# Optimization experiments

Measured on AMD Instinct MI355X. Metric: run time of the kernel, lower is better.

The kernel has to match this reference:

```python
import jax, jax.numpy as jnp
import numpy as np

D_MODEL = 1024
N_HEADS = 16
D_HEAD = D_MODEL // N_HEADS
D_FF = 4096
BATCH = 2
SEQ = 2048
EPS = 1e-5


def setup_inputs() -> dict:
    key = jax.random.key(0)
    ks = jax.random.split(key, 8)
    s = 0.02
    x = jax.random.normal(ks[0], (BATCH, SEQ, D_MODEL), dtype=jnp.float32)
    # Per-head projection weights, stacked: [H, d_head, d_model] (torch Linear stores (out,in))
    wq = jax.random.normal(ks[1], (N_HEADS, D_HEAD, D_MODEL), dtype=jnp.float32) * s
    wk = jax.random.normal(ks[2], (N_HEADS, D_HEAD, D_MODEL), dtype=jnp.float32) * s
    wv = jax.random.normal(ks[3], (N_HEADS, D_HEAD, D_MODEL), dtype=jnp.float32) * s
    wo = jax.random.normal(ks[4], (D_MODEL, D_MODEL), dtype=jnp.float32) * s
    w1 = jax.random.normal(ks[5], (D_FF, D_MODEL), dtype=jnp.float32) * s
    w2 = jax.random.normal(ks[6], (D_MODEL, D_FF), dtype=jnp.float32) * s
    ln1_g = jnp.ones((D_MODEL,), jnp.float32)
    ln1_b = jnp.zeros((D_MODEL,), jnp.float32)
    ln2_g = jnp.ones((D_MODEL,), jnp.float32)
    ln2_b = jnp.zeros((D_MODEL,), jnp.float32)
    return {"x": x, "wq": wq, "wk": wk, "wv": wv, "wo": wo,
            "w1": w1, "w2": w2, "ln1_g": ln1_g, "ln1_b": ln1_b,
            "ln2_g": ln2_g, "ln2_b": ln2_b}


def _layer_norm(x, g, b):
    mu = jnp.mean(x, axis=-1, keepdims=True)
    var = jnp.mean(jnp.square(x - mu), axis=-1, keepdims=True)
    return (x - mu) * jax.lax.rsqrt(var + EPS) * g + b


def _mha(h, wq, wk, wv, wo):
    # h: [b,s,d]; wq/wk/wv: [H,dh,d] -> q/k/v: [b,H,s,dh]
    q = jnp.einsum('bsd,hed->bhse', h, wq)
    k = jnp.einsum('bsd,hed->bhse', h, wk)
    v = jnp.einsum('bsd,hed->bhse', h, wv)
    scores = jnp.einsum('bhqe,bhke->bhqk', q, k) / jnp.sqrt(jnp.float32(D_HEAD))
    weights = jax.nn.softmax(scores, axis=-1)
    ctx = jnp.einsum('bhqk,bhke->bhqe', weights, v)  # [b,H,s,dh]
    # concat heads in order (head 0 first) -> [b,s,H*dh]
    concat = jnp.transpose(ctx, (0, 2, 1, 3)).reshape(h.shape[0], h.shape[1], D_MODEL)
    return concat @ wo.T


def reference(x, wq, wk, wv, wo, w1, w2, ln1_g, ln1_b, ln2_g, ln2_b):
    h = _layer_norm(x, ln1_g, ln1_b)
    attn_out = _mha(h, wq, wk, wv, wo)
    h2 = _layer_norm(x + attn_out, ln2_g, ln2_b)
    ff = jax.nn.gelu(h2 @ w1.T, approximate=False) @ w2.T
    return x + ff
```

## Files before the change

kernel.cpp:

```cpp
#include <hip/hip_runtime.h>
#include <hip/hip_bf16.h>
#include <math.h>

typedef __bf16 bf16_t;
typedef __bf16 bf16x8 __attribute__((ext_vector_type(8)));
typedef __bf16 bf16x4 __attribute__((ext_vector_type(4)));
typedef float f32x4 __attribute__((ext_vector_type(4)));
typedef unsigned int u32;
typedef u32 u32x2 __attribute__((ext_vector_type(2)));

#define DM 1024
#define SEQL 2048
#define NTOK 4096
#define QKVN 3072

__device__ __forceinline__ void gload_lds16(const bf16_t* g, bf16_t* l){
  __builtin_amdgcn_global_load_lds((const __attribute__((address_space(1))) void*)g,
                                   (__attribute__((address_space(3))) void*)l, 16, 0, 0);
}
__device__ __forceinline__ u32 ldsoff(const void* p){
  return (u32)(size_t)(__attribute__((address_space(3))) const void*)p;
}
__device__ __forceinline__ u32x2 tr64(u32 byte_off){
  u32x2 d;
  asm volatile("ds_read_b64_tr_b16 %0, %1" : "=v"(d) : "v"(byte_off));
  return d;
}
__device__ __forceinline__ u32 pack2(float a, float b){
  union{ __bf16 h[2]; u32 w; } z;
  z.h[0]=(__bf16)a; z.h[1]=(__bf16)b; return z.w;
}

__global__ __launch_bounds__(256) void prep_kernel(
    const float* __restrict__ wq, const float* __restrict__ wk,
    const float* __restrict__ wv, const float* __restrict__ wo,
    const float* __restrict__ w1, const float* __restrict__ w2,
    const float* __restrict__ x,  const float* __restrict__ g1,
    const float* __restrict__ b1,
    bf16_t* __restrict__ wqkv_b, bf16_t* __restrict__ wo_b,
    bf16_t* __restrict__ w1_b,   bf16_t* __restrict__ w2_b,
    bf16_t* __restrict__ h1)
{
  __shared__ float red[8];
  const int bid = blockIdx.x;
  const int t = threadIdx.x;
  if (bid < 12288){
    const int flat = (bid*256 + t)*4;
    const int seg = flat >> 20;
    const int off1m = flat & 1048575;
    const float* src; bf16_t* dst;
    if (seg < 3){
      src = (seg==0 ? wq : (seg==1 ? wk : wv)) + off1m;
      dst = wqkv_b + flat;
    } else if (seg == 3){
      src = wo + off1m;  dst = wo_b + off1m;
    } else if (seg < 8){
      src = w1 + (flat - 4*1048576);  dst = w1_b + (flat - 4*1048576);
    } else {
      src = w2 + (flat - 8*1048576);  dst = w2_b + (flat - 8*1048576);
    }
    const float4 v = *(const float4*)src;
    bf16x4 o; o[0]=(__bf16)v.x; o[1]=(__bf16)v.y; o[2]=(__bf16)v.z; o[3]=(__bf16)v.w;
    *(bf16x4*)dst = o;
  } else {
    const int row = bid - 12288;
    const float4 v = *(const float4*)(x + (size_t)row*DM + t*4);
    float s  = v.x+v.y+v.z+v.w;
    float sq = v.x*v.x+v.y*v.y+v.z*v.z+v.w*v.w;
    #pragma unroll
    for (int m=1;m<64;m<<=1){ s += __shfl_xor(s,m); sq += __shfl_xor(sq,m); }
    const int w = t>>6;
    if ((t&63)==0){ red[w]=s; red[4+w]=sq; }
    __syncthreads();
    s  = red[0]+red[1]+red[2]+red[3];
    sq = red[4]+red[5]+red[6]+red[7];
    const float mean = s*(1.f/DM);
    const float var  = sq*(1.f/DM) - mean*mean;
    const float rstd = rsqrtf(var + 1e-5f);
    const float4 gg = *(const float4*)(g1 + t*4);
    const float4 bb = *(const float4*)(b1 + t*4);
    bf16x4 o;
    o[0]=(__bf16)((v.x-mean)*rstd*gg.x+bb.x);
    o[1]=(__bf16)((v.y-mean)*rstd*gg.y+bb.y);
    o[2]=(__bf16)((v.z-mean)*rstd*gg.z+bb.z);
    o[3]=(__bf16)((v.w-mean)*rstd*gg.w+bb.w);
    *(bf16x4*)(h1 + (size_t)row*DM + t*4) = o;
  }
}

__global__ __launch_bounds__(256) void ln_kernel(const float* __restrict__ in,
    const float* __restrict__ g, const float* __restrict__ bta,
    bf16_t* __restrict__ outp)
{
  const int row = blockIdx.x;
  const int t = threadIdx.x;
  const float4 v = *(const float4*)(in + (size_t)row*DM + t*4);
  float s  = v.x+v.y+v.z+v.w;
  float sq = v.x*v.x+v.y*v.y+v.z*v.z+v.w*v.w;
  #pragma unroll
  for (int m=1;m<64;m<<=1){ s += __shfl_xor(s,m); sq += __shfl_xor(sq,m); }
  __shared__ float red[8];
  const int w = t>>6;
  if ((t&63)==0){ red[w]=s; red[4+w]=sq; }
  __syncthreads();
  s  = red[0]+red[1]+red[2]+red[3];
  sq = red[4]+red[5]+red[6]+red[7];
  const float mean = s*(1.f/DM);
  const float var  = sq*(1.f/DM) - mean*mean;
  const float rstd = rsqrtf(var + 1e-5f);
  const float4 gg = *(const float4*)(g + t*4);
  const float4 bb = *(const float4*)(bta + t*4);
  bf16x4 o;
  o[0]=(__bf16)((v.x-mean)*rstd*gg.x+bb.x);
  o[1]=(__bf16)((v.y-mean)*rstd*gg.y+bb.y);
  o[2]=(__bf16)((v.z-mean)*rstd*gg.z+bb.z);
  o[3]=(__bf16)((v.w-mean)*rstd*gg.w+bb.w);
  *(bf16x4*)(outp + (size_t)row*DM + t*4) = o;
}

template<int EPI>
__global__ __launch_bounds__(512, 2) void gemm8ph(
    const bf16_t* __restrict__ A, const bf16_t* __restrict__ Bw,
    void* __restrict__ Cout, int N, int K)
{
  __shared__ __align__(16) char ldsb[131072];
  const int tid = threadIdx.x, lane = tid&63, wid = tid>>6;
  const int q16 = lane&15, g = lane>>4;
  const int wm = wid>>2, wn = wid&3;

  const int flat = blockIdx.y*gridDim.x + blockIdx.x;
  const int xcd = flat&7, jj = flat>>3;
  const int NY = gridDim.y;
  const int jdiv = jj/NY, jmod = jj - jdiv*NY;
  const int bm = (xcd*2 + jdiv)*256, bn = jmod*256;

  int mloc, kloc;
  {
    const u32 L = tid*16;
    const u32 logical = L ^ (((L>>9)&1)<<5);
    mloc = (int)(logical>>6);
    kloc = (int)((logical&63)>>1);
  }
  const bf16_t* asrc = A  + (size_t)(bm + mloc)*K + kloc;
  const bf16_t* bsrc = Bw + (size_t)(bn + mloc)*K + kloc;
  const u32 laneOff = ((u32)(q16*64 + g*16)) ^ ((u32)(q16&8)<<2);

  f32x4 acc[8][4] = {};
  bf16x8 bv[4];

  auto stage = [&](int buf, int kh, int isB, int s){
    const bf16_t* src = isB ? bsrc : asrc;
    #pragma unroll
    for (int h2=0; h2<2; h2++)
      gload_lds16(src + (size_t)(h2*128)*K + s*64 + kh*32,
                  (bf16_t*)(ldsb + buf*65536 + isB*32768 + kh*16384 + h2*8192 + tid*16));
  };

  stage(0,0,0,0); stage(0,0,1,0); stage(0,1,0,0); stage(0,1,1,0);
  stage(1,0,0,1); stage(1,0,1,1);
  asm volatile("s_waitcnt vmcnt(4)" ::: "memory");
  __builtin_amdgcn_s_barrier();

  const int NSTEP = K>>6;
  const int NIT = NSTEP>>1;

#define PHASE(BUF,KH,MH,DOST,SBUF,SKH,SISB,SSTEP,CK) { \
    bf16x8 av[4]; \
    const char* Ab_ = ldsb + (BUF)*65536 + (KH)*16384 + wm*8192; \
    _Pragma("unroll") for (int jx=0;jx<4;jx++) \
      av[jx] = *(const bf16x8*)(Ab_ + (((MH)*4+jx)<<10) + laneOff); \
    if ((MH)==0){ \
      const char* Bb_ = ldsb + (BUF)*65536 + 32768 + (KH)*16384 + (wn>>1)*8192; \
      _Pragma("unroll") for (int jx=0;jx<4;jx++) \
        bv[jx] = *(const bf16x8*)(Bb_ + ((((wn&1)*4)+jx)<<10) + laneOff); \
    } \
    if (DOST) stage(SBUF,SKH,SISB,SSTEP); \
    asm volatile("s_barrier" ::: "memory"); \
    asm volatile("s_waitcnt lgkmcnt(0)" ::: "memory"); \
    __builtin_amdgcn_s_setprio(1); \
    _Pragma("unroll") for (int jx=0;jx<4;jx++) \
      _Pragma("unroll") for (int j2=0;j2<4;j2++) \
        acc[(MH)*4+jx][j2] = __builtin_amdgcn_mfma_f32_16x16x32_bf16(av[jx], bv[j2], acc[(MH)*4+jx][j2],0,0,0); \
    __builtin_amdgcn_s_setprio(0); \
    if (CK){ if (nl) { asm volatile("s_waitcnt vmcnt(4)" ::: "memory"); } \
             else    { asm volatile("s_waitcnt vmcnt(0)" ::: "memory"); } } \
    asm volatile("s_barrier" ::: "memory"); }

  for (int it=0; it<NIT; it++){
    const int s0 = 2*it, s1 = s0+1;
    const bool nl = (it+1 < NIT);
    PHASE(0,0,0, 1,  1,1,0, s1,   0)
    PHASE(0,0,1, 1,  1,1,1, s1,   0)
    PHASE(0,1,0, nl, 0,0,0, s0+2, 0)
    PHASE(0,1,1, nl, 0,0,1, s0+2, 1)
    PHASE(1,0,0, nl, 0,1,0, s0+2, 0)
    PHASE(1,0,1, nl, 0,1,1, s0+2, 0)
    PHASE(1,1,0, nl, 1,0,0, s1+2, 0)
    PHASE(1,1,1, nl, 1,0,1, s1+2, 1)
  }
#undef PHASE

  #pragma unroll
  for (int fm=0; fm<8; fm++)
    #pragma unroll
    for (int fn=0; fn<4; fn++)
      #pragma unroll
      for (int i=0; i<4; i++){
        const int r = bm + wm*128 + fm*16 + g*4 + i;
        const int c = bn + wn*64 + fn*16 + q16;
        const size_t idx = (size_t)r*N + c;
        const float vv = acc[fm][fn][i];
        if constexpr (EPI==0){
          ((bf16_t*)Cout)[idx] = (__bf16)vv;
        } else {
          const float ge = 0.5f*vv*(1.0f + erff(vv*0.70710678118654752f));
          ((bf16_t*)Cout)[idx] = (__bf16)ge;
        }
      }
}

__global__ __launch_bounds__(512, 2) void gemm128(
    const bf16_t* __restrict__ A, const bf16_t* __restrict__ Bw,
    float* __restrict__ Cout, const float* __restrict__ X,
    int N, int K)
{
  constexpr int BK = 32;
  __shared__ __align__(16) char ldsb[3*16384];
  const int tid = threadIdx.x, lane = tid&63, wid = tid>>6;
  const int q16 = lane&15, g = lane>>4;
  const int wm = wid>>2, wn = wid&3;

  const int flat = blockIdx.y*gridDim.x + blockIdx.x;
  const int xcd = flat&7, j = flat>>3;
  const int bm = ((xcd<<2) + (j>>3))*128, bn = (j&7)*128;

  int mloc, kloc;
  {
    const u32 L = tid*16;
    const u32 logical = L ^ (((L>>9)&1)<<5);
    mloc = (int)(logical>>6);
    kloc = (int)((logical&63)>>1);
  }
  const bf16_t* asrc = A  + (size_t)(bm + mloc)*K + kloc;
  const bf16_t* bsrc = Bw + (size_t)(bn + mloc)*K + kloc;
  const u32 laneOff = ((u32)(q16*64 + g*16)) ^ ((u32)(q16&8)<<2);

  f32x4 acc[4][2] = {};

  auto stageA = [&](int buf, int k0){
    gload_lds16(asrc + k0, (bf16_t*)(ldsb + buf*16384 + tid*16));
  };
  auto stageB = [&](int buf, int k0){
    gload_lds16(bsrc + k0, (bf16_t*)(ldsb + buf*16384 + 8192 + tid*16));
  };

  stageA(0,0); stageB(0,0);
  stageA(1,BK); stageB(1,BK);
  asm volatile("s_waitcnt vmcnt(2)" ::: "memory");
  __builtin_amdgcn_s_barrier();

  const int NT = K/BK;
  int bcur = 0;
  for (int kt=0; kt<NT; kt++){
    const int bstg = (bcur >= 1) ? bcur-1 : bcur+2;
    const char* Ab = ldsb + bcur*16384 + wm*4096;
    const char* Bb = ldsb + bcur*16384 + 8192 + wn*2048;
    const bool sOK = (kt+2 < NT);
    const int k0s = (kt+2)*BK;
    bf16x8 bv[2];
    #pragma unroll
    for (int p=0; p<2; p++){
      bf16x8 av[2];
      #pragma unroll
      for (int jx=0;jx<2;jx++)
        av[jx] = *(const bf16x8*)(Ab + ((p*2+jx)<<10) + laneOff);
      if (p==0){
        #pragma unroll
        for (int jx=0;jx<2;jx++)
          bv[jx] = *(const bf16x8*)(Bb + (jx<<10) + laneOff);
      }
      if (sOK){
        if (p==0) stageA(bstg,k0s);
        else      stageB(bstg,k0s);
      }
      asm volatile("s_barrier" ::: "memory");
      __builtin_amdgcn_s_setprio(1);
      #pragma unroll
      for (int jx=0;jx<2;jx++)
        #pragma unroll
        for (int j2=0;j2<2;j2++)
          acc[p*2+jx][j2] = __builtin_amdgcn_mfma_f32_16x16x32_bf16(av[jx], bv[j2], acc[p*2+jx][j2], 0,0,0);
      __builtin_amdgcn_s_setprio(0);
      if (p==1){
        if (sOK) asm volatile("s_waitcnt vmcnt(2)" ::: "memory");
        else     asm volatile("s_waitcnt vmcnt(0)" ::: "memory");
      }
      asm volatile("s_barrier" ::: "memory");
    }
    bcur = (bcur==2)?0:bcur+1;
  }

  #pragma unroll
  for (int fm=0; fm<4; fm++)
    #pragma unroll
    for (int fn=0; fn<2; fn++)
      #pragma unroll
      for (int i=0; i<4; i++){
        const int r = bm + wm*64 + fm*16 + g*4 + i;
        const int c = bn + wn*32 + fn*16 + q16;
        const size_t idx = (size_t)r*N + c;
        Cout[idx] = X[idx] + acc[fm][fn][i];
      }
}

__global__ __launch_bounds__(512, 4) void attn_kernel(
    const bf16_t* __restrict__ QKV, bf16_t* __restrict__ Ctx)
{
  __shared__ __align__(16) bf16_t Ks[2][64*64];
  __shared__ __align__(16) bf16_t Vs[2][16*4*72];
  const int tid = threadIdx.x, lane = tid&63, w = tid>>6;
  const int g = lane>>4, q16 = lane&15;
  const int bh = blockIdx.y, b = bh>>4, h = bh&15;
  const int qr0 = blockIdx.x*128 + w*16;
  const size_t tok0 = (size_t)b*SEQL;
  const int ch0 = h*64;

  bf16x8 aq[2];
  #pragma unroll
  for (int ks=0; ks<2; ks++){
    bf16x8 t = *(const bf16x8*)(QKV + (tok0+qr0+q16)*QKVN + ch0 + ks*32 + g*8);
    #pragma unroll
    for (int jx=0;jx<8;jx++) t[jx] = (__bf16)((float)t[jx]*0.125f);
    aq[ks] = t;
  }

  const int srow = tid>>3, sc8 = (tid&7)*8;
  const bf16_t* kptr = QKV + (tok0+srow)*QKVN + 1024 + ch0 + sc8;
  const bf16_t* vptr = kptr + 1024;
  const int kwoff = srow*64 + (sc8 ^ ((srow&7)<<3));
  const int vwoff = ((srow>>2)*4 + (sc8>>4))*72 + (srow&3)*16 + (sc8&15);

  float mrun = -1e30f, lrun = 0.f;
  f32x4 o[4] = {};

  bf16x8 kreg = *(const bf16x8*)kptr;
  bf16x8 vreg = *(const bf16x8*)vptr;
  *(bf16x8*)&Ks[0][kwoff] = kreg;
  *(bf16x8*)&Vs[0][vwoff] = vreg;
  kreg = *(const bf16x8*)(kptr + (size_t)64*QKVN);
  vreg = *(const bf16x8*)(vptr + (size_t)64*QKVN);

  const int NT = SEQL/64;
  for (int t=0; t<NT; t++){
    __syncthreads();
    if (t+1 < NT){
      *(bf16x8*)&Ks[(t+1)&1][kwoff] = kreg;
      *(bf16x8*)&Vs[(t+1)&1][vwoff] = vreg;
      if (t+2 < NT){
        kreg = *(const bf16x8*)(kptr + (size_t)(t+2)*64*QKVN);
        vreg = *(const bf16x8*)(vptr + (size_t)(t+2)*64*QKVN);
      }
    }
    const bf16_t* ksb = Ks[t&1];
    const u32 vs0 = ldsoff(&Vs[t&1][0]);

    f32x4 s[4] = {};
    #pragma unroll
    for (int ks=0; ks<2; ks++){
      #pragma unroll
      for (int fn=0; fn<4; fn++){
        const int r = fn*16 + q16;
        const int ce = ks*32 + g*8;
        bf16x8 bk = *(const bf16x8*)&ksb[r*64 + (ce ^ ((r&7)<<3))];
        s[fn] = __builtin_amdgcn_mfma_f32_16x16x32_bf16(bk, aq[ks], s[fn], 0, 0, 0);
      }
    }

    float m0 = fmaxf(fmaxf(s[0][0],s[0][1]), fmaxf(s[0][2],s[0][3]));
    float m1 = fmaxf(fmaxf(s[1][0],s[1][1]), fmaxf(s[1][2],s[1][3]));
    float m2 = fmaxf(fmaxf(s[2][0],s[2][1]), fmaxf(s[2][2],s[2][3]));
    float m3 = fmaxf(fmaxf(s[3][0],s[3][1]), fmaxf(s[3][2],s[3][3]));
    float mx = fmaxf(fmaxf(m0,m1), fmaxf(m2,m3));
    mx = fmaxf(mx, __shfl_xor(mx,16));
    mx = fmaxf(mx, __shfl_xor(mx,32));

    if (!__all(mx <= mrun + 8.0f)){
      const float mnew = fmaxf(mrun, mx);
      const float alpha = __expf(mrun - mnew);
      #pragma unroll
      for (int i=0;i<4;i++){
        const float ai = __shfl(alpha, g*4+i);
        o[0][i]*=ai; o[1][i]*=ai; o[2][i]*=ai; o[3][i]*=ai;
      }
      lrun *= alpha;
      mrun = mnew;
    }

    float rs = 0.f;
    u32 u[4][2];
    #pragma unroll
    for (int fn=0; fn<4; fn++){
      const float e0=__expf(s[fn][0]-mrun), e1=__expf(s[fn][1]-mrun);
      const float e2=__expf(s[fn][2]-mrun), e3=__expf(s[fn][3]-mrun);
      rs += (e0+e1)+(e2+e3);
      u[fn][0] = pack2(e0,e1);
      u[fn][1] = pack2(e2,e3);
    }
    rs += __shfl_xor(rs,16);
    rs += __shfl_xor(rs,32);
    lrun += rs;

    #pragma unroll
    for (int ks=0; ks<2; ks++){
      u32x2 vlo[4], vhi[4];
      #pragma unroll
      for (int ne=0; ne<4; ne++){
        const u32 vb = vs0 + (u32)((((ks*8 + 2*g)*4 + ne)*72 + q16)*2);
        vlo[ne] = tr64(vb);
        vhi[ne] = tr64(vb + 576);
      }
      union { u32 wd[4]; bf16x8 v; } pa;
      #pragma unroll
      for (int jj=0; jj<4; jj++){
        const int src = q16 + ((((g&1)<<1) + (jj>>1))<<4);
        const u32 a0 = (u32)__shfl((int)u[2*ks  ][jj&1], src);
        const u32 a1 = (u32)__shfl((int)u[2*ks+1][jj&1], src);
        pa.wd[jj] = (g&2) ? a1 : a0;
      }
      asm volatile("s_waitcnt lgkmcnt(0)" ::: "memory");
      __builtin_amdgcn_sched_barrier(0);
      union { u32x2 u2[2]; bf16x8 v; } cc;
      #pragma unroll
      for (int ne=0; ne<4; ne++){
        cc.u2[0]=vlo[ne]; cc.u2[1]=vhi[ne];
        o[ne] = __builtin_amdgcn_mfma_f32_16x16x32_bf16(pa.v, cc.v, o[ne], 0, 0, 0);
      }
    }
  }

  const float rl = 1.0f/lrun;
  #pragma unroll
  for (int i=0; i<4; i++){
    const float ri = __shfl(rl, g*4+i);
    #pragma unroll
    for (int ne=0; ne<4; ne++){
      const int r = qr0 + g*4 + i;
      Ctx[(tok0+r)*DM + ch0 + ne*16 + q16] = (__bf16)(o[ne][i]*ri);
    }
  }
}

extern "C" void kernel_launch(void* const* d_in, const int* in_sizes, int n_in,
                              void* d_out, int out_size, void* d_ws, size_t ws_size,
                              hipStream_t stream)
{
  (void)in_sizes; (void)n_in; (void)out_size; (void)ws_size;
  const float* x  = (const float*)d_in[0];
  const float* wq = (const float*)d_in[1];
  const float* wk = (const float*)d_in[2];
  const float* wv = (const float*)d_in[3];
  const float* wo = (const float*)d_in[4];
  const float* w1 = (const float*)d_in[5];
  const float* w2 = (const float*)d_in[6];
  const float* g1 = (const float*)d_in[7];
  const float* b1 = (const float*)d_in[8];
  const float* g2 = (const float*)d_in[9];
  const float* b2 = (const float*)d_in[10];
  float* out = (float*)d_out;
  char* ws = (char*)d_ws;
  const size_t MB = 1024ull*1024ull;

  bf16_t* wqkv_b = (bf16_t*)(ws);
  bf16_t* wo_b   = (bf16_t*)(ws + 6*MB);
  bf16_t* w1_b   = (bf16_t*)(ws + 8*MB);
  bf16_t* w2_b   = (bf16_t*)(ws + 16*MB);
  bf16_t* h1     = (bf16_t*)(ws + 24*MB);
  bf16_t* qkv    = (bf16_t*)(ws + 32*MB);
  bf16_t* ctx    = (bf16_t*)(ws + 56*MB);
  float*  res2   = (float*)(ws + 64*MB);
  bf16_t* h2     = h1;
  bf16_t* ffm    = (bf16_t*)(ws + 32*MB);

  prep_kernel<<<16384, 256, 0, stream>>>(wq, wk, wv, wo, w1, w2, x, g1, b1,
                                         wqkv_b, wo_b, w1_b, w2_b, h1);
  gemm8ph<0><<<dim3(16, 12), 512, 0, stream>>>(h1, wqkv_b, (void*)qkv, QKVN, 1024);
  attn_kernel<<<dim3(16, 32), 512, 0, stream>>>(qkv, ctx);
  gemm128<<<dim3(32, 8), 512, 0, stream>>>(ctx, wo_b, res2, x, 1024, 1024);
  ln_kernel<<<NTOK, 256, 0, stream>>>(res2, g2, b2, h2);
  gemm8ph<2><<<dim3(16, 16), 512, 0, stream>>>(h2, w1_b, (void*)ffm, 4096, 1024);
  gemm128<<<dim3(32, 8), 512, 0, stream>>>(ffm, w2_b, out, x, 1024, 4096);
}
```

Before: 247.2 us.

## Store residual in bf16, load K tiles via direct LDS DMA, use exp2 softmax

The out-projection GEMM now writes the residual sum x+attn as bf16, and the second layernorm reads bf16, which halves that intermediate's memory traffic. The attention kernel moves K tiles with global_load_lds straight into pre-swizzled LDS instead of staging them in registers. It also folds log2(e) into the Q scale so the softmax can use exp2f, with the rescale threshold adjusted to match. The cost is bf16 rounding of the residual before LN2, which slightly lowers accuracy.

```diff
diff --git a/kernel.cpp b/kernel.cpp
--- a/kernel.cpp
+++ b/kernel.cpp
@@ -88,13 +88,15 @@
   }
 }
 
-__global__ __launch_bounds__(256) void ln_kernel(const float* __restrict__ in,
+__global__ __launch_bounds__(256) void lnb_kernel(const bf16_t* __restrict__ in,
     const float* __restrict__ g, const float* __restrict__ bta,
     bf16_t* __restrict__ outp)
 {
   const int row = blockIdx.x;
   const int t = threadIdx.x;
-  const float4 v = *(const float4*)(in + (size_t)row*DM + t*4);
+  const bf16x4 raw = *(const bf16x4*)(in + (size_t)row*DM + t*4);
+  float4 v;
+  v.x=(float)raw[0]; v.y=(float)raw[1]; v.z=(float)raw[2]; v.w=(float)raw[3];
   float s  = v.x+v.y+v.z+v.w;
   float sq = v.x*v.x+v.y*v.y+v.z*v.z+v.w*v.w;
   #pragma unroll
@@ -219,9 +221,10 @@
       }
 }
 
+template<int EPI>
 __global__ __launch_bounds__(512, 2) void gemm128(
     const bf16_t* __restrict__ A, const bf16_t* __restrict__ Bw,
-    float* __restrict__ Cout, const float* __restrict__ X,
+    void* __restrict__ Cout, const float* __restrict__ X,
     int N, int K)
 {
   constexpr int BK = 32;
@@ -309,7 +312,9 @@
         const int r = bm + wm*64 + fm*16 + g*4 + i;
         const int c = bn + wn*32 + fn*16 + q16;
         const size_t idx = (size_t)r*N + c;
-        Cout[idx] = X[idx] + acc[fm][fn][i];
+        const float vv = X[idx] + acc[fm][fn][i];
+        if constexpr (EPI==0) ((bf16_t*)Cout)[idx] = (__bf16)vv;
+        else                  ((float*)Cout)[idx] = vv;
       }
 }
 
@@ -330,36 +335,31 @@
   for (int ks=0; ks<2; ks++){
     bf16x8 t = *(const bf16x8*)(QKV + (tok0+qr0+q16)*QKVN + ch0 + ks*32 + g*8);
     #pragma unroll
-    for (int jx=0;jx<8;jx++) t[jx] = (__bf16)((float)t[jx]*0.125f);
+    for (int jx=0;jx<8;jx++) t[jx] = (__bf16)((float)t[jx]*0.18033688f);
     aq[ks] = t;
   }
 
   const int srow = tid>>3, sc8 = (tid&7)*8;
-  const bf16_t* kptr = QKV + (tok0+srow)*QKVN + 1024 + ch0 + sc8;
-  const bf16_t* vptr = kptr + 1024;
-  const int kwoff = srow*64 + (sc8 ^ ((srow&7)<<3));
+  const bf16_t* kptr_swz = QKV + (tok0+srow)*QKVN + 1024 + ch0 + (sc8 ^ ((srow&7)<<3));
+  const bf16_t* vptr = QKV + (tok0+srow)*QKVN + 2048 + ch0 + sc8;
   const int vwoff = ((srow>>2)*4 + (sc8>>4))*72 + (srow&3)*16 + (sc8&15);
 
   float mrun = -1e30f, lrun = 0.f;
   f32x4 o[4] = {};
 
-  bf16x8 kreg = *(const bf16x8*)kptr;
+  gload_lds16(kptr_swz, &Ks[0][tid*8]);
   bf16x8 vreg = *(const bf16x8*)vptr;
-  *(bf16x8*)&Ks[0][kwoff] = kreg;
   *(bf16x8*)&Vs[0][vwoff] = vreg;
-  kreg = *(const bf16x8*)(kptr + (size_t)64*QKVN);
   vreg = *(const bf16x8*)(vptr + (size_t)64*QKVN);
 
   const int NT = SEQL/64;
   for (int t=0; t<NT; t++){
     __syncthreads();
     if (t+1 < NT){
-      *(bf16x8*)&Ks[(t+1)&1][kwoff] = kreg;
+      gload_lds16(kptr_swz + (size_t)(t+1)*64*QKVN, &Ks[(t+1)&1][tid*8]);
       *(bf16x8*)&Vs[(t+1)&1][vwoff] = vreg;
-      if (t+2 < NT){
-        kreg = *(const bf16x8*)(kptr + (size_t)(t+2)*64*QKVN);
+      if (t+2 < NT)
         vreg = *(const bf16x8*)(vptr + (size_t)(t+2)*64*QKVN);
-      }
     }
     const bf16_t* ksb = Ks[t&1];
     const u32 vs0 = ldsoff(&Vs[t&1][0]);
@@ -384,9 +384,9 @@
     mx = fmaxf(mx, __shfl_xor(mx,16));
     mx = fmaxf(mx, __shfl_xor(mx,32));
 
-    if (!__all(mx <= mrun + 8.0f)){
+    if (!__all(mx <= mrun + 11.54f)){
       const float mnew = fmaxf(mrun, mx);
-      const float alpha = __expf(mrun - mnew);
+      const float alpha = exp2f(mrun - mnew);
       #pragma unroll
       for (int i=0;i<4;i++){
         const float ai = __shfl(alpha, g*4+i);
@@ -400,8 +400,8 @@
     u32 u[4][2];
     #pragma unroll
     for (int fn=0; fn<4; fn++){
-      const float e0=__expf(s[fn][0]-mrun), e1=__expf(s[fn][1]-mrun);
-      const float e2=__expf(s[fn][2]-mrun), e3=__expf(s[fn][3]-mrun);
+      const float e0=exp2f(s[fn][0]-mrun), e1=exp2f(s[fn][1]-mrun);
+      const float e2=exp2f(s[fn][2]-mrun), e3=exp2f(s[fn][3]-mrun);
       rs += (e0+e1)+(e2+e3);
       u[fn][0] = pack2(e0,e1);
       u[fn][1] = pack2(e2,e3);
@@ -477,7 +477,7 @@
   bf16_t* h1     = (bf16_t*)(ws + 24*MB);
   bf16_t* qkv    = (bf16_t*)(ws + 32*MB);
   bf16_t* ctx    = (bf16_t*)(ws + 56*MB);
-  float*  res2   = (float*)(ws + 64*MB);
+  bf16_t* res2b  = (bf16_t*)(ws + 64*MB);
   bf16_t* h2     = h1;
   bf16_t* ffm    = (bf16_t*)(ws + 32*MB);
 
@@ -485,8 +485,8 @@
                                          wqkv_b, wo_b, w1_b, w2_b, h1);
   gemm8ph<0><<<dim3(16, 12), 512, 0, stream>>>(h1, wqkv_b, (void*)qkv, QKVN, 1024);
   attn_kernel<<<dim3(16, 32), 512, 0, stream>>>(qkv, ctx);
-  gemm128<<<dim3(32, 8), 512, 0, stream>>>(ctx, wo_b, res2, x, 1024, 1024);
-  ln_kernel<<<NTOK, 256, 0, stream>>>(res2, g2, b2, h2);
+  gemm128<0><<<dim3(32, 8), 512, 0, stream>>>(ctx, wo_b, (void*)res2b, x, 1024, 1024);
+  lnb_kernel<<<NTOK, 256, 0, stream>>>(res2b, g2, b2, h2);
   gemm8ph<2><<<dim3(16, 16), 512, 0, stream>>>(h2, w1_b, (void*)ffm, 4096, 1024);
-  gemm128<<<dim3(32, 8), 512, 0, stream>>>(ffm, w2_b, out, x, 1024, 4096);
-}
+  gemm128<1><<<dim3(32, 8), 512, 0, stream>>>(ffm, w2_b, (void*)out, x, 1024, 4096);
+}
```

New measurement: 258.5 us. 1.05x slower.
